# Kernel tuning notes

Measured on AMD Instinct MI355X. Metric: run time of the kernel, lower is better.

## Reference

```python
import jax, jax.numpy as jnp
import numpy as np

N = 4096      # n_nodes
F = 512       # input_dim
R = 64        # repr_dim
H = 8         # n_heads
EPS_BIAS = 0.01
ALPHA = 0.2   # LeakyReLU negative slope
NEG_BIG = 1e16


def setup_inputs() -> dict:
    key = jax.random.key(0)
    k1, k2, k3, k4, k5 = jax.random.split(key, 5)
    node_matrix = jax.random.normal(k1, (N, F), dtype=jnp.float32)
    adjacency_matrix = (jax.random.uniform(k2, (N, N)) < 0.01).astype(jnp.float32)
    adjacency_matrix = jnp.maximum(adjacency_matrix, jnp.eye(N, dtype=jnp.float32))
    # learned parameters (xavier-ish scale)
    W = jax.random.normal(k3, (H, F, R), dtype=jnp.float32) * 0.06
    shared_attention = jax.random.normal(k4, (H, 2 * R), dtype=jnp.float32) * 0.1
    attention_biases = jax.random.normal(k5, (N, N), dtype=jnp.float32) * 0.02
    return {
        "node_matrix": node_matrix,
        "adjacency_matrix": adjacency_matrix,
        "W": W,
        "shared_attention": shared_attention,
        "attention_biases": attention_biases,
    }


def reference(node_matrix, adjacency_matrix, W, shared_attention, attention_biases):
    # hidden_repr: [H, N, R]
    hidden = jnp.einsum('nf,hfr->hnr', node_matrix, W)
    # per-head source/destination scores: [H, N]
    a_src = jnp.einsum('hnr,hr->hn', hidden, shared_attention[:, :R])
    a_dst = jnp.einsum('hnr,hr->hn', hidden, shared_attention[:, R:])
    # broadcast-sum + trainable pair bias: [H, N, N]
    pre = a_src[:, :, None] + a_dst[:, None, :] + EPS_BIAS * attention_biases[None]
    full = jnp.where(pre >= 0, pre, ALPHA * pre)  # LeakyReLU
    # adjacency masking then row softmax
    scores = full + (-NEG_BIG * (1.0 - adjacency_matrix))[None]
    att = jax.nn.softmax(scores, axis=-1)  # [H, N, N]
    # weighted aggregation: [H, N, R]
    out = jnp.einsum('hnm,hmr->hnr', att, hidden)
    # 'concat' aggregation: [N, H*R], head h occupies columns h*R:(h+1)*R
    return jnp.transpose(out, (1, 0, 2)).reshape(N, H * R)
```

## Files before the change

kernel.cpp:

```cpp
#include <hip/hip_runtime.h>
#include <hip/hip_bf16.h>

#define NN 4096
#define FF 512
#define RR 64
#define HH 8
#define HR (HH * RR)
#define CAP 128
#define ATT_STRIDE 144

typedef short bf16x8 __attribute__((ext_vector_type(8)));
typedef float f32x4 __attribute__((ext_vector_type(4)));

__device__ __forceinline__ unsigned short f2bf(float f) {
  __hip_bfloat16 h = __float2bfloat16(f);
  return *reinterpret_cast<unsigned short*>(&h);
}
__device__ __forceinline__ float bf2f(unsigned short u) {
  union { unsigned u32; float f; } cv;
  cv.u32 = ((unsigned)u) << 16;
  return cv.f;
}
__device__ __forceinline__ unsigned nib4(const float4 v) {
  unsigned m = 0;
  if (v.x != 0.f) m |= 1u;
  if (v.y != 0.f) m |= 2u;
  if (v.z != 0.f) m |= 4u;
  if (v.w != 0.f) m |= 8u;
  return m;
}

__global__ __launch_bounds__(256) void k_stream(
    const float* __restrict__ X, const float* __restrict__ W,
    const float* __restrict__ adj,
    unsigned short* __restrict__ Xb, unsigned short* __restrict__ BbT,
    int* __restrict__ colsG, int* __restrict__ cnts)
{
  __shared__ unsigned short wt[64][68];
  const int b = blockIdx.x;
  const int tid = threadIdx.x;

  if (b < 1024) {
    const int lane = tid & 63;
    const int row = b * 4 + (tid >> 6);
    const float* arow = adj + (size_t)row * NN;
    unsigned long long pm = 0;
    {
      float4 buf[8];
#pragma unroll
      for (int c = 0; c < 8; ++c)
        buf[c] = *reinterpret_cast<const float4*>(&arow[c * 256 + (lane << 2)]);
#pragma unroll
      for (int c = 0; c < 8; ++c)
        pm |= (unsigned long long)nib4(buf[c]) << (4 * c);
#pragma unroll
      for (int c = 0; c < 8; ++c)
        buf[c] = *reinterpret_cast<const float4*>(&arow[(c + 8) * 256 + (lane << 2)]);
#pragma unroll
      for (int c = 0; c < 8; ++c)
        pm |= (unsigned long long)nib4(buf[c]) << (4 * c + 32);
    }
    const int cnt = __popcll(pm);
    int pfx = cnt;
#pragma unroll
    for (int off = 1; off < 64; off <<= 1) {
      const int o = __shfl_up(pfx, off);
      if (lane >= off) pfx += o;
    }
    int pos = pfx - cnt;
    unsigned long long m = pm;
    int* cg = colsG + (size_t)row * CAP;
    while (m) {
      const int bit = (int)__builtin_ctzll(m);
      m &= m - 1;
      if (pos < CAP) cg[pos] = ((bit >> 2) << 8) + (lane << 2) + (bit & 3);
      ++pos;
    }
    if (lane == 63) cnts[row] = pfx < CAP ? pfx : CAP;
  } else if (b < 3072) {
    const int t = (b - 1024) * 256 + tid;
    const float4 v = reinterpret_cast<const float4*>(X)[t];
    ushort4 u;
    u.x = f2bf(v.x); u.y = f2bf(v.y); u.z = f2bf(v.z); u.w = f2bf(v.w);
    reinterpret_cast<ushort4*>(Xb)[t] = u;
  } else {
    const int b2 = b - 3072;
    const int h = b2 >> 3;
    const int f0 = (b2 & 7) << 6;
    const int fr = tid >> 2;
    const int rq = (tid & 3) << 4;
    const float* wp = W + (size_t)h * FF * RR + (size_t)(f0 + fr) * RR + rq;
#pragma unroll
    for (int v = 0; v < 4; ++v) {
      const float4 x = *reinterpret_cast<const float4*>(wp + v * 4);
      wt[rq + v * 4 + 0][fr] = f2bf(x.x);
      wt[rq + v * 4 + 1][fr] = f2bf(x.y);
      wt[rq + v * 4 + 2][fr] = f2bf(x.z);
      wt[rq + v * 4 + 3][fr] = f2bf(x.w);
    }
    __syncthreads();
    const int r = tid >> 2;
    unsigned short* op = BbT + (size_t)(h * 64 + r) * FF + f0 + ((tid & 3) << 4);
    int4 w0, w1;
    w0 = *reinterpret_cast<const int4*>(&wt[r][(tid & 3) << 4]);
    w1 = *reinterpret_cast<const int4*>(&wt[r][((tid & 3) << 4) + 8]);
    *reinterpret_cast<int4*>(op) = w0;
    *reinterpret_cast<int4*>(op + 8) = w1;
  }
}

__global__ __launch_bounds__(256) void k_gemm_hidden(
    const unsigned short* __restrict__ Xb,
    const unsigned short* __restrict__ BbT,
    const float* __restrict__ sa,
    unsigned short* __restrict__ hiddenT,
    float* __restrict__ a_src,
    float* __restrict__ a_dstT)
{
  const int row0 = blockIdx.x * 64;
  const int h = blockIdx.y;
  const int n0 = h * 64;
  __shared__ unsigned short Als[64 * 32];
  __shared__ unsigned short Bls[64 * 32];
  __shared__ float redS[64][2];
  __shared__ float redD[64][2];
  const int tid = threadIdx.x;
  const int l = tid & 63;
  const int wid = tid >> 6;
  const int wr = wid >> 1, wc = wid & 1;

  f32x4 acc[2][2];
#pragma unroll
  for (int a = 0; a < 2; ++a)
#pragma unroll
    for (int bb = 0; bb < 2; ++bb) acc[a][bb] = (f32x4){0.f, 0.f, 0.f, 0.f};

  const int srow = tid >> 2;
  const int skel = (tid & 3) * 8;

  for (int k0 = 0; k0 < FF; k0 += 32) {
    const int4 av = *reinterpret_cast<const int4*>(
        &Xb[(size_t)(row0 + srow) * FF + k0 + skel]);
    const int4 bv = *reinterpret_cast<const int4*>(
        &BbT[(size_t)(n0 + srow) * FF + k0 + skel]);
    __syncthreads();
    *reinterpret_cast<int4*>(&Als[tid * 8]) = av;
    *reinterpret_cast<int4*>(&Bls[tid * 8]) = bv;
    __syncthreads();

    const int ka = (l >> 4) * 8;
    const bf16x8 a0 = *reinterpret_cast<const bf16x8*>(&Als[(32 * wr + 0  + (l & 15)) * 32 + ka]);
    const bf16x8 a1 = *reinterpret_cast<const bf16x8*>(&Als[(32 * wr + 16 + (l & 15)) * 32 + ka]);
    const bf16x8 b0 = *reinterpret_cast<const bf16x8*>(&Bls[(32 * wc + 0  + (l & 15)) * 32 + ka]);
    const bf16x8 b1 = *reinterpret_cast<const bf16x8*>(&Bls[(32 * wc + 16 + (l & 15)) * 32 + ka]);
    acc[0][0] = __builtin_amdgcn_mfma_f32_16x16x32_bf16(a0, b0, acc[0][0], 0, 0, 0);
    acc[0][1] = __builtin_amdgcn_mfma_f32_16x16x32_bf16(a0, b1, acc[0][1], 0, 0, 0);
    acc[1][0] = __builtin_amdgcn_mfma_f32_16x16x32_bf16(a1, b0, acc[1][0], 0, 0, 0);
    acc[1][1] = __builtin_amdgcn_mfma_f32_16x16x32_bf16(a1, b1, acc[1][1], 0, 0, 0);
  }

  const int lg = l >> 4;
  const int lc = l & 15;

#pragma unroll
  for (int mi = 0; mi < 2; ++mi)
#pragma unroll
    for (int ni = 0; ni < 2; ++ni)
#pragma unroll
      for (int j = 0; j < 4; ++j) {
        const int rowg = row0 + 32 * wr + 16 * mi + (lg << 2) + j;
        const int colg = n0 + 32 * wc + 16 * ni + lc;
        hiddenT[(size_t)rowg * HR + colg] = f2bf(acc[mi][ni][j]);
      }

  float sS[2], sD[2];
#pragma unroll
  for (int ni = 0; ni < 2; ++ni) {
    const int col = 32 * wc + 16 * ni + lc;
    sS[ni] = sa[(size_t)h * 2 * RR + col];
    sD[ni] = sa[(size_t)h * 2 * RR + RR + col];
  }
#pragma unroll
  for (int mi = 0; mi < 2; ++mi)
#pragma unroll
    for (int j = 0; j < 4; ++j) {
      float ps = acc[mi][0][j] * sS[0] + acc[mi][1][j] * sS[1];
      float pd = acc[mi][0][j] * sD[0] + acc[mi][1][j] * sD[1];
#pragma unroll
      for (int off = 8; off >= 1; off >>= 1) {
        ps += __shfl_xor(ps, off);
        pd += __shfl_xor(pd, off);
      }
      if (lc == 0) {
        const int rl = 32 * wr + 16 * mi + (lg << 2) + j;
        redS[rl][wc] = ps;
        redD[rl][wc] = pd;
      }
    }
  __syncthreads();
  if (tid < 64) {
    a_src[(size_t)h * NN + row0 + tid] = redS[tid][0] + redS[tid][1];
    a_dstT[(size_t)(row0 + tid) * HH + h] = redD[tid][0] + redD[tid][1];
  }
}

__global__ __launch_bounds__(256) void k_gat_row(
    const int* __restrict__ colsG,
    const int* __restrict__ cnts,
    const float* __restrict__ bias,
    const float* __restrict__ a_src,
    const float* __restrict__ a_dstT,
    const unsigned short* __restrict__ hiddenT,
    float* __restrict__ out)
{
  const int i = blockIdx.x;
  const int tid = threadIdx.x;

  __shared__ __align__(16) float att[HH][ATT_STRIDE];
  __shared__ int cols[CAP];
  __shared__ __align__(16) float accred[2][HR];

  const int count = cnts[i];
  const float* brow = bias + (size_t)i * NN;

  float asrc[HH];
#pragma unroll
  for (int h = 0; h < HH; ++h) asrc[h] = a_src[(size_t)h * NN + i];

  if (tid < count) {
    const int c = colsG[(size_t)i * CAP + tid];
    cols[tid] = c;
    const float b = 0.01f * brow[c];
    const float4 d0 = *reinterpret_cast<const float4*>(&a_dstT[(size_t)c * HH]);
    const float4 d1 = *reinterpret_cast<const float4*>(&a_dstT[(size_t)c * HH + 4]);
    float s;
    s = asrc[0] + d0.x + b; att[0][tid] = (s >= 0.f) ? s : 0.2f * s;
    s = asrc[1] + d0.y + b; att[1][tid] = (s >= 0.f) ? s : 0.2f * s;
    s = asrc[2] + d0.z + b; att[2][tid] = (s >= 0.f) ? s : 0.2f * s;
    s = asrc[3] + d0.w + b; att[3][tid] = (s >= 0.f) ? s : 0.2f * s;
    s = asrc[4] + d1.x + b; att[4][tid] = (s >= 0.f) ? s : 0.2f * s;
    s = asrc[5] + d1.y + b; att[5][tid] = (s >= 0.f) ? s : 0.2f * s;
    s = asrc[6] + d1.z + b; att[6][tid] = (s >= 0.f) ? s : 0.2f * s;
    s = asrc[7] + d1.w + b; att[7][tid] = (s >= 0.f) ? s : 0.2f * s;
  }
  __syncthreads();

  {
    const int g = tid >> 5;
    const int l = tid & 31;
    float* arow_h = att[g];
    float m = -3.0e38f;
    for (int t = l; t < count; t += 32) m = fmaxf(m, arow_h[t]);
#pragma unroll
    for (int o = 16; o >= 1; o >>= 1) m = fmaxf(m, __shfl_xor(m, o));
    float ssum = 0.f;
    for (int t = l; t < count; t += 32) {
      const float e = expf(arow_h[t] - m);
      arow_h[t] = e;
      ssum += e;
    }
#pragma unroll
    for (int o = 16; o >= 1; o >>= 1) ssum += __shfl_xor(ssum, o);
    const float inv = 1.0f / ssum;
    for (int t = l; t < count; t += 32) arow_h[t] *= inv;
  }
  __syncthreads();

  {
    const int g2 = tid >> 7;
    const int o0 = (tid & 127) << 2;
    const float* attrow = att[o0 >> 6];
    const unsigned short* hb = hiddenT + o0;
    const int half = (count + 1) >> 1;
    const int t0 = g2 * half;
    const int t1 = (g2 == 0) ? half : count;
    float4 acc = make_float4(0.f, 0.f, 0.f, 0.f);
    int t = t0;
    for (; t + 2 <= t1; t += 2) {
      const int ca = cols[t], cb = cols[t + 1];
      const float aa = attrow[t], ab = attrow[t + 1];
      const ushort4 ua = *reinterpret_cast<const ushort4*>(hb + (size_t)ca * HR);
      const ushort4 ub = *reinterpret_cast<const ushort4*>(hb + (size_t)cb * HR);
      acc.x += aa * bf2f(ua.x) + ab * bf2f(ub.x);
      acc.y += aa * bf2f(ua.y) + ab * bf2f(ub.y);
      acc.z += aa * bf2f(ua.z) + ab * bf2f(ub.z);
      acc.w += aa * bf2f(ua.w) + ab * bf2f(ub.w);
    }
    if (t < t1) {
      const int c = cols[t];
      const float a = attrow[t];
      const ushort4 u = *reinterpret_cast<const ushort4*>(hb + (size_t)c * HR);
      acc.x += a * bf2f(u.x); acc.y += a * bf2f(u.y);
      acc.z += a * bf2f(u.z); acc.w += a * bf2f(u.w);
    }
    *reinterpret_cast<float4*>(&accred[g2][o0]) = acc;
  }
  __syncthreads();
  {
    const int o = tid << 1;
    const float2 r = make_float2(accred[0][o] + accred[1][o],
                                 accred[0][o + 1] + accred[1][o + 1]);
    *reinterpret_cast<float2*>(&out[(size_t)i * HR + o]) = r;
  }
}

extern "C" void kernel_launch(void* const* d_in, const int* in_sizes, int n_in,
                              void* d_out, int out_size, void* d_ws, size_t ws_size,
                              hipStream_t stream) {
  const float* X    = (const float*)d_in[0];
  const float* adj  = (const float*)d_in[1];
  const float* W    = (const float*)d_in[2];
  const float* sa   = (const float*)d_in[3];
  const float* bias = (const float*)d_in[4];
  float* out = (float*)d_out;

  unsigned short* hiddenT = (unsigned short*)d_ws;
  unsigned short* Xb  = hiddenT + (size_t)NN * HR;
  unsigned short* BbT = Xb + (size_t)NN * FF;
  float* a_src  = (float*)(BbT + (size_t)HR * FF);
  float* a_dstT = a_src + (size_t)HH * NN;
  int* cnts     = (int*)(a_dstT + (size_t)NN * HH);
  int* colsG    = cnts + NN;

  k_stream<<<dim3(3136), 256, 0, stream>>>(X, W, adj, Xb, BbT, colsG, cnts);
  k_gemm_hidden<<<dim3(NN / 64, HH), 256, 0, stream>>>(Xb, BbT, sa, hiddenT, a_src, a_dstT);
  k_gat_row<<<dim3(NN), 256, 0, stream>>>(colsG, cnts, bias, a_src, a_dstT, hiddenT, out);
}
```

Baseline: 48.20 us.

## Transpose a_src, zero-pad column lists, and split aggregation four ways

a_src is now stored node-major so each row block reads its eight head scores with two float4 loads instead of eight strided scalar loads. Column lists are zero-padded to CAP, which lets the row kernel issue its index, bias and a_dst loads unconditionally for the first 128 threads before the count is known, hiding some of the load latency. The aggregation phase now uses four thread groups, each handling eight output columns over a quarter of the neighbours, and the partial sums are reduced in shared memory. In exchange, the k_stream kernel does extra padding stores and the row kernel reads padded entries whose results are never used.

```diff
diff --git a/kernel.cpp b/kernel.cpp
--- a/kernel.cpp
+++ b/kernel.cpp
@@ -76,7 +76,9 @@
       if (pos < CAP) cg[pos] = ((bit >> 2) << 8) + (lane << 2) + (bit & 3);
       ++pos;
     }
-    if (lane == 63) cnts[row] = pfx < CAP ? pfx : CAP;
+    const int tot = __shfl(pfx, 63);
+    for (int p = tot + lane; p < CAP; p += 64) cg[p] = 0;
+    if (lane == 63) cnts[row] = tot < CAP ? tot : CAP;
   } else if (b < 3072) {
     const int t = (b - 1024) * 256 + tid;
     const float4 v = reinterpret_cast<const float4*>(X)[t];
@@ -101,9 +103,8 @@
     __syncthreads();
     const int r = tid >> 2;
     unsigned short* op = BbT + (size_t)(h * 64 + r) * FF + f0 + ((tid & 3) << 4);
-    int4 w0, w1;
-    w0 = *reinterpret_cast<const int4*>(&wt[r][(tid & 3) << 4]);
-    w1 = *reinterpret_cast<const int4*>(&wt[r][((tid & 3) << 4) + 8]);
+    int4 w0 = *reinterpret_cast<const int4*>(&wt[r][(tid & 3) << 4]);
+    int4 w1 = *reinterpret_cast<const int4*>(&wt[r][((tid & 3) << 4) + 8]);
     *reinterpret_cast<int4*>(op) = w0;
     *reinterpret_cast<int4*>(op + 8) = w1;
   }
@@ -114,7 +115,7 @@
     const unsigned short* __restrict__ BbT,
     const float* __restrict__ sa,
     unsigned short* __restrict__ hiddenT,
-    float* __restrict__ a_src,
+    float* __restrict__ a_srcT,
     float* __restrict__ a_dstT)
 {
   const int row0 = blockIdx.x * 64;
@@ -199,7 +200,7 @@
     }
   __syncthreads();
   if (tid < 64) {
-    a_src[(size_t)h * NN + row0 + tid] = redS[tid][0] + redS[tid][1];
+    a_srcT[(size_t)(row0 + tid) * HH + h] = redS[tid][0] + redS[tid][1];
     a_dstT[(size_t)(row0 + tid) * HH + h] = redD[tid][0] + redD[tid][1];
   }
 }
@@ -208,7 +209,7 @@
     const int* __restrict__ colsG,
     const int* __restrict__ cnts,
     const float* __restrict__ bias,
-    const float* __restrict__ a_src,
+    const float* __restrict__ a_srcT,
     const float* __restrict__ a_dstT,
     const unsigned short* __restrict__ hiddenT,
     float* __restrict__ out)
@@ -218,30 +219,34 @@
 
   __shared__ __align__(16) float att[HH][ATT_STRIDE];
   __shared__ int cols[CAP];
-  __shared__ __align__(16) float accred[2][HR];
-
+  __shared__ __align__(16) float accred[4][HR];
+
+  int c = 0;
+  float4 d0, d1;
+  float b = 0.f;
+  if (tid < CAP) {
+    c = colsG[(size_t)i * CAP + tid];
+  }
   const int count = cnts[i];
-  const float* brow = bias + (size_t)i * NN;
-
-  float asrc[HH];
-#pragma unroll
-  for (int h = 0; h < HH; ++h) asrc[h] = a_src[(size_t)h * NN + i];
-
-  if (tid < count) {
-    const int c = colsG[(size_t)i * CAP + tid];
+  if (tid < CAP) {
+    b = 0.01f * bias[(size_t)i * NN + c];
+    d0 = *reinterpret_cast<const float4*>(&a_dstT[(size_t)c * HH]);
+    d1 = *reinterpret_cast<const float4*>(&a_dstT[(size_t)c * HH + 4]);
+  }
+  const float4 s0 = *reinterpret_cast<const float4*>(&a_srcT[(size_t)i * HH]);
+  const float4 s1 = *reinterpret_cast<const float4*>(&a_srcT[(size_t)i * HH + 4]);
+
+  if (tid < CAP) {
     cols[tid] = c;
-    const float b = 0.01f * brow[c];
-    const float4 d0 = *reinterpret_cast<const float4*>(&a_dstT[(size_t)c * HH]);
-    const float4 d1 = *reinterpret_cast<const float4*>(&a_dstT[(size_t)c * HH + 4]);
     float s;
-    s = asrc[0] + d0.x + b; att[0][tid] = (s >= 0.f) ? s : 0.2f * s;
-    s = asrc[1] + d0.y + b; att[1][tid] = (s >= 0.f) ? s : 0.2f * s;
-    s = asrc[2] + d0.z + b; att[2][tid] = (s >= 0.f) ? s : 0.2f * s;
-    s = asrc[3] + d0.w + b; att[3][tid] = (s >= 0.f) ? s : 0.2f * s;
-    s = asrc[4] + d1.x + b; att[4][tid] = (s >= 0.f) ? s : 0.2f * s;
-    s = asrc[5] + d1.y + b; att[5][tid] = (s >= 0.f) ? s : 0.2f * s;
-    s = asrc[6] + d1.z + b; att[6][tid] = (s >= 0.f) ? s : 0.2f * s;
-    s = asrc[7] + d1.w + b; att[7][tid] = (s >= 0.f) ? s : 0.2f * s;
+    s = s0.x + d0.x + b; att[0][tid] = (s >= 0.f) ? s : 0.2f * s;
+    s = s0.y + d0.y + b; att[1][tid] = (s >= 0.f) ? s : 0.2f * s;
+    s = s0.z + d0.z + b; att[2][tid] = (s >= 0.f) ? s : 0.2f * s;
+    s = s0.w + d0.w + b; att[3][tid] = (s >= 0.f) ? s : 0.2f * s;
+    s = s1.x + d1.x + b; att[4][tid] = (s >= 0.f) ? s : 0.2f * s;
+    s = s1.y + d1.y + b; att[5][tid] = (s >= 0.f) ? s : 0.2f * s;
+    s = s1.z + d1.z + b; att[6][tid] = (s >= 0.f) ? s : 0.2f * s;
+    s = s1.w + d1.w + b; att[7][tid] = (s >= 0.f) ? s : 0.2f * s;
   }
   __syncthreads();
 
@@ -267,39 +272,34 @@
   __syncthreads();
 
   {
-    const int g2 = tid >> 7;
-    const int o0 = (tid & 127) << 2;
+    const int g2 = tid >> 6;
+    const int o0 = (tid & 63) << 3;
     const float* attrow = att[o0 >> 6];
     const unsigned short* hb = hiddenT + o0;
-    const int half = (count + 1) >> 1;
-    const int t0 = g2 * half;
-    const int t1 = (g2 == 0) ? half : count;
-    float4 acc = make_float4(0.f, 0.f, 0.f, 0.f);
-    int t = t0;
-    for (; t + 2 <= t1; t += 2) {
-      const int ca = cols[t], cb = cols[t + 1];
-      const float aa = attrow[t], ab = attrow[t + 1];
-      const ushort4 ua = *reinterpret_cast<const ushort4*>(hb + (size_t)ca * HR);
-      const ushort4 ub = *reinterpret_cast<const ushort4*>(hb + (size_t)cb * HR);
-      acc.x += aa * bf2f(ua.x) + ab * bf2f(ub.x);
-      acc.y += aa * bf2f(ua.y) + ab * bf2f(ub.y);
-      acc.z += aa * bf2f(ua.z) + ab * bf2f(ub.z);
-      acc.w += aa * bf2f(ua.w) + ab * bf2f(ub.w);
-    }
-    if (t < t1) {
-      const int c = cols[t];
+    const int q = (count + 3) >> 2;
+    const int t0 = g2 * q;
+    const int t1 = min(t0 + q, count);
+    float4 accA = make_float4(0.f, 0.f, 0.f, 0.f);
+    float4 accB = make_float4(0.f, 0.f, 0.f, 0.f);
+    for (int t = t0; t < t1; ++t) {
+      const int cc = cols[t];
       const float a = attrow[t];
-      const ushort4 u = *reinterpret_cast<const ushort4*>(hb + (size_t)c * HR);
-      acc.x += a * bf2f(u.x); acc.y += a * bf2f(u.y);
-      acc.z += a * bf2f(u.z); acc.w += a * bf2f(u.w);
-    }
-    *reinterpret_cast<float4*>(&accred[g2][o0]) = acc;
+      const ushort4 ua = *reinterpret_cast<const ushort4*>(hb + (size_t)cc * HR);
+      const ushort4 ub = *reinterpret_cast<const ushort4*>(hb + (size_t)cc * HR + 4);
+      accA.x += a * bf2f(ua.x); accA.y += a * bf2f(ua.y);
+      accA.z += a * bf2f(ua.z); accA.w += a * bf2f(ua.w);
+      accB.x += a * bf2f(ub.x); accB.y += a * bf2f(ub.y);
+      accB.z += a * bf2f(ub.z); accB.w += a * bf2f(ub.w);
+    }
+    *reinterpret_cast<float4*>(&accred[g2][o0]) = accA;
+    *reinterpret_cast<float4*>(&accred[g2][o0 + 4]) = accB;
   }
   __syncthreads();
   {
     const int o = tid << 1;
-    const float2 r = make_float2(accred[0][o] + accred[1][o],
-                                 accred[0][o + 1] + accred[1][o + 1]);
+    const float2 r = make_float2(
+        accred[0][o] + accred[1][o] + accred[2][o] + accred[3][o],
+        accred[0][o + 1] + accred[1][o + 1] + accred[2][o + 1] + accred[3][o + 1]);
     *reinterpret_cast<float2*>(&out[(size_t)i * HR + o]) = r;
   }
 }
@@ -317,12 +317,12 @@
   unsigned short* hiddenT = (unsigned short*)d_ws;
   unsigned short* Xb  = hiddenT + (size_t)NN * HR;
   unsigned short* BbT = Xb + (size_t)NN * FF;
-  float* a_src  = (float*)(BbT + (size_t)HR * FF);
-  float* a_dstT = a_src + (size_t)HH * NN;
+  float* a_srcT = (float*)(BbT + (size_t)HR * FF);
+  float* a_dstT = a_srcT + (size_t)NN * HH;
   int* cnts     = (int*)(a_dstT + (size_t)NN * HH);
   int* colsG    = cnts + NN;
 
   k_stream<<<dim3(3136), 256, 0, stream>>>(X, W, adj, Xb, BbT, colsG, cnts);
-  k_gemm_hidden<<<dim3(NN / 64, HH), 256, 0, stream>>>(Xb, BbT, sa, hiddenT, a_src, a_dstT);
-  k_gat_row<<<dim3(NN), 256, 0, stream>>>(colsG, cnts, bias, a_src, a_dstT, hiddenT, out);
-}
+  k_gemm_hidden<<<dim3(NN / 64, HH), 256, 0, stream>>>(Xb, BbT, sa, hiddenT, a_srcT, a_dstT);
+  k_gat_row<<<dim3(NN), 256, 0, stream>>>(colsG, cnts, bias, a_srcT, a_dstT, hiddenT, out);
+}
```

New measurement: 47.00 us. 2.5% less time.
